# Kernel tuning notes

Measured on AMD Instinct MI355X. Metric: run time of the kernel, lower is better.

Reference implementation:

```python
import jax, jax.numpy as jnp
import numpy as np

D = 256        # d_model
H = 8          # n_heads
L = 4          # n_layers
DFF = 1024     # d_ff = 4*d_model
T = 32768      # total_doms
B = 64         # batch_size (events)
MAX_DOMS = 768 # fixed padded sequence length
NSENS = 5160   # IceCube sensor count


def _layernorm(x, w, b):
    m = x.mean(-1, keepdims=True)
    v = ((x - m) ** 2).mean(-1, keepdims=True)
    return (x - m) * jax.lax.rsqrt(v + 1e-5) * w + b


def _forward(dom_embeddings, geometry, geo_w1, geo_b1, geo_w2, geo_b2,
             qkv_w, qkv_b, out_w, out_b, ln1_w, ln1_b, ln2_w, ln2_b,
             ffn_w1, ffn_b1, ffn_w2, ffn_b2,
             head_w1, head_b1, head_w2, head_b2,
             dom_ids, dom_to_event_idx, batch_size):
    # geometry-aware positional encoding
    geo = geometry[dom_ids] / 500.0                                   # (T,3)
    ge = jax.nn.gelu(geo @ geo_w1.T + geo_b1, approximate=False) @ geo_w2.T + geo_b2
    feat = dom_embeddings + ge                                        # (T,D)

    # pack ragged events -> padded (B, MAX_DOMS, D); dom_to_event_idx is sorted
    total = feat.shape[0]
    counts = jax.ops.segment_sum(jnp.ones((total,), jnp.int32),
                                 dom_to_event_idx, num_segments=batch_size)
    offsets = jnp.cumsum(counts) - counts                              # exclusive prefix
    pos = jnp.arange(total, dtype=jnp.int32) - offsets[dom_to_event_idx]
    x = jnp.zeros((batch_size, MAX_DOMS, D), feat.dtype).at[dom_to_event_idx, pos].set(feat)
    valid = jnp.zeros((batch_size, MAX_DOMS), bool).at[dom_to_event_idx, pos].set(True)
    pad = ~valid                                                       # True for padding

    hd = D // H
    scale = 1.0 / np.sqrt(hd)
    for l in range(L):  # pre-LN transformer encoder (norm_first=True, relu FFN)
        h = _layernorm(x, ln1_w[l], ln1_b[l])
        qkv = h @ qkv_w[l].T + qkv_b[l]                                # (B,S,3D)
        q, k, v = jnp.split(qkv, 3, axis=-1)
        q = q.reshape(batch_size, MAX_DOMS, H, hd)
        k = k.reshape(batch_size, MAX_DOMS, H, hd)
        v = v.reshape(batch_size, MAX_DOMS, H, hd)
        sc = jnp.einsum('bqhd,bkhd->bhqk', q, k) * scale
        sc = jnp.where(pad[:, None, None, :], -1e9, sc)
        a = jax.nn.softmax(sc, axis=-1)
        o = jnp.einsum('bhqk,bkhd->bqhd', a, v).reshape(batch_size, MAX_DOMS, D)
        x = x + o @ out_w[l].T + out_b[l]
        h2 = _layernorm(x, ln2_w[l], ln2_b[l])
        x = x + jax.nn.relu(h2 @ ffn_w1[l].T + ffn_b1[l]) @ ffn_w2[l].T + ffn_b2[l]

    # masked mean pooling
    m = valid[..., None].astype(x.dtype)
    emb = (x * m).sum(axis=1) / jnp.clip(m.sum(axis=1), 1.0)           # (B,D)

    # prediction head + L2 normalization to unit vector
    vec = jax.nn.relu(emb @ head_w1.T + head_b1) @ head_w2.T + head_b2  # (B,3)
    norm = jnp.sqrt(jnp.sum(vec ** 2, axis=1, keepdims=True))
    return vec / (norm + 1e-8)


def setup_inputs() -> dict:
    key = jax.random.key(0)
    ks = jax.random.split(key, 24)
    s = 0.02
    z = jnp.zeros
    inp = {
        'dom_embeddings': jax.random.normal(ks[0], (T, D), jnp.float32),
        'geometry': jax.random.normal(ks[1], (NSENS, 3), jnp.float32) * 300.0,
        'geo_w1': jax.random.normal(ks[2], (D // 2, 3), jnp.float32) * s,
        'geo_b1': z((D // 2,), jnp.float32),
        'geo_w2': jax.random.normal(ks[3], (D, D // 2), jnp.float32) * s,
        'geo_b2': z((D,), jnp.float32),
        'qkv_w': jax.random.normal(ks[4], (L, 3 * D, D), jnp.float32) * s,
        'qkv_b': z((L, 3 * D), jnp.float32),
        'out_w': jax.random.normal(ks[5], (L, D, D), jnp.float32) * s,
        'out_b': z((L, D), jnp.float32),
        'ln1_w': jnp.ones((L, D), jnp.float32), 'ln1_b': z((L, D), jnp.float32),
        'ln2_w': jnp.ones((L, D), jnp.float32), 'ln2_b': z((L, D), jnp.float32),
        'ffn_w1': jax.random.normal(ks[6], (L, DFF, D), jnp.float32) * s,
        'ffn_b1': z((L, DFF), jnp.float32),
        'ffn_w2': jax.random.normal(ks[7], (L, D, DFF), jnp.float32) * s,
        'ffn_b2': z((L, D), jnp.float32),
        'head_w1': jax.random.normal(ks[8], (D, D), jnp.float32) * s,
        'head_b1': z((D,), jnp.float32),
        'head_w2': jax.random.normal(ks[9], (3, D), jnp.float32) * s,
        'head_b2': z((3,), jnp.float32),
        'dom_ids': jax.random.randint(ks[10], (T,), 0, NSENS, jnp.int32),
        'dom_to_event_idx': jnp.sort(jax.random.randint(ks[11], (T,), 0, B, jnp.int32)),
        'batch_size': B,
    }
    return inp


def reference(dom_embeddings, geometry, geo_w1, geo_b1, geo_w2, geo_b2,
              qkv_w, qkv_b, out_w, out_b, ln1_w, ln1_b, ln2_w, ln2_b,
              ffn_w1, ffn_b1, ffn_w2, ffn_b2,
              head_w1, head_b1, head_w2, head_b2,
              dom_ids, dom_to_event_idx, batch_size):
    return _forward(dom_embeddings, geometry, geo_w1, geo_b1, geo_w2, geo_b2,
                    qkv_w, qkv_b, out_w, out_b, ln1_w, ln1_b, ln2_w, ln2_b,
                    ffn_w1, ffn_b1, ffn_w2, ffn_b2,
                    head_w1, head_b1, head_w2, head_b2,
                    dom_ids, dom_to_event_idx, batch_size)
```

## Files before the change

kernel.cpp:

```cpp
#include <hip/hip_runtime.h>
#include <stdint.h>

typedef unsigned short u16;
typedef uint32_t u32;
typedef __bf16 bf16x8 __attribute__((ext_vector_type(8)));
typedef float f32x4 __attribute__((ext_vector_type(4)));

constexpr int T_ = 32768, D_ = 256, H_ = 8, L_ = 4, B_ = 64, NSENS_ = 5160;
constexpr int MGEO_ = 5248;

template <bool Bv> struct bconst { static constexpr bool value = Bv; };

__device__ __forceinline__ u16 f2b(float f) {
  uint32_t u = __builtin_bit_cast(uint32_t, f);
  u += 0x7fffu + ((u >> 16) & 1u);
  return (u16)(u >> 16);
}
__device__ __forceinline__ float fexp2(float x) {
  float r;
  asm("v_exp_f32 %0, %1" : "=v"(r) : "v"(x));
  return r;
}
__device__ __forceinline__ u32 cvtpk(float lo, float hi) {
  u32 r;
  asm("v_cvt_pk_bf16_f32 %0, %1, %2" : "=v"(r) : "v"(lo), "v"(hi));
  return r;
}

__device__ __forceinline__ void gload16(const void* g, void* l) {
  __builtin_amdgcn_global_load_lds(
      (const __attribute__((address_space(1))) void*)g,
      (__attribute__((address_space(3))) void*)l, 16, 0, 0);
}

__global__ void k_offsets(const int* __restrict__ d2e, int* __restrict__ offs) {
  int t = threadIdx.x;
  if (t > B_) return;
  int lo = 0, hi = T_;
  while (lo < hi) { int mid = (lo + hi) >> 1; if (d2e[mid] < t) lo = mid + 1; else hi = mid; }
  offs[t] = lo;
}

__global__ void k_f2b(const float* __restrict__ s, u16* __restrict__ d, int n) {
  int i = blockIdx.x * blockDim.x + threadIdx.x;
  int str = gridDim.x * blockDim.x;
  for (; i < n; i += str) d[i] = f2b(s[i]);
}

__global__ void k_geo1(const float* __restrict__ geom, const float* __restrict__ w1,
                       const float* __restrict__ b1, u16* __restrict__ h1) {
  int i = blockIdx.x * blockDim.x + threadIdx.x;
  if (i >= NSENS_ * 128) return;
  int s = i >> 7, c = i & 127;
  float g0 = geom[s * 3 + 0] * (1.0f / 500.0f);
  float g1 = geom[s * 3 + 1] * (1.0f / 500.0f);
  float g2 = geom[s * 3 + 2] * (1.0f / 500.0f);
  float a = g0 * w1[c * 3 + 0] + g1 * w1[c * 3 + 1] + g2 * w1[c * 3 + 2] + b1[c];
  float g = 0.5f * a * (1.0f + erff(a * 0.70710678118654752f));
  h1[i] = f2b(g);
}

__global__ void k_feat(const float4* __restrict__ de, const float4* __restrict__ ge,
                       const int* __restrict__ dom_ids, float4* __restrict__ x) {
  int i = blockIdx.x * blockDim.x + threadIdx.x;
  if (i >= T_ * 64) return;
  int row = i >> 6, c = i & 63;
  int sid = dom_ids[row];
  float4 a = de[i];
  float4 b = ge[sid * 64 + c];
  float4 o;
  o.x = a.x + b.x; o.y = a.y + b.y; o.z = a.z + b.z; o.w = a.w + b.w;
  x[i] = o;
}

__global__ void k_ln(const float* __restrict__ x, const float* __restrict__ w,
                     const float* __restrict__ b, u16* __restrict__ h) {
  int row = blockIdx.x * 4 + (threadIdx.x >> 6);
  int lane = threadIdx.x & 63;
  const float4 v = *(const float4*)(x + (size_t)row * 256 + lane * 4);
  float s = v.x + v.y + v.z + v.w;
  float q = v.x * v.x + v.y * v.y + v.z * v.z + v.w * v.w;
#pragma unroll
  for (int m = 1; m < 64; m <<= 1) { s += __shfl_xor(s, m); q += __shfl_xor(q, m); }
  float mean = s * (1.0f / 256.0f);
  float var = fmaxf(q * (1.0f / 256.0f) - mean * mean, 0.0f);
  float rs = 1.0f / sqrtf(var + 1e-5f);
  float4 wv = *(const float4*)(w + lane * 4);
  float4 bv = *(const float4*)(b + lane * 4);
  ushort4 o;
  o.x = f2b((v.x - mean) * rs * wv.x + bv.x);
  o.y = f2b((v.y - mean) * rs * wv.y + bv.y);
  o.z = f2b((v.z - mean) * rs * wv.z + bv.z);
  o.w = f2b((v.w - mean) * rs * wv.w + bv.w);
  *(ushort4*)(h + (size_t)row * 256 + lane * 4) = o;
}

template <int EPI>
__global__ __launch_bounds__(256) void k_gemm(const u16* __restrict__ A, const u16* __restrict__ W,
                                              const float* __restrict__ bias, void* __restrict__ out,
                                              int M, int N, int K, int NXB) {
  __shared__ __align__(16) u16 lds[4 * 8192];
  const int nb = gridDim.x;
  const int id = blockIdx.x;
  const int gid = ((nb & 7) == 0) ? ((id & 7) * (nb >> 3) + (id >> 3)) : id;
  const int by = gid / NXB, bx = gid % NXB;
  const int m0 = by * 128, n0 = bx * 128;
  const int tid = threadIdx.x, lane = tid & 63, wv = tid >> 6;
  const int wr = wv >> 1, wc = wv & 1;
  const int l16 = lane & 15, lhi = lane >> 4;
  f32x4 acc[4][4] = {};
  const int NK = K >> 6;

  auto stage = [&](int buf, int kt) {
    char* lbase = (char*)lds + buf * 32768;
#pragma unroll
    for (int c = 0; c < 4; ++c) {
      int pb = c * 4096 + wv * 1024;
      int p = pb + lane * 16;
      int o = p ^ (((p >> 9) & 1) << 5);
      int row = o >> 7, colb = o & 127;
      gload16((const char*)A + ((size_t)(m0 + row) * K) * 2 + kt * 128 + colb, lbase + pb);
      gload16((const char*)W + ((size_t)(n0 + row) * K) * 2 + kt * 128 + colb,
              lbase + 16384 + pb);
    }
  };
  auto compute = [&](int buf) {
    const char* la = (const char*)lds + buf * 32768;
    const char* lb = la + 16384;
#pragma unroll
    for (int ks = 0; ks < 2; ++ks) {
      bf16x8 af[4], bfr[4];
#pragma unroll
      for (int i = 0; i < 4; ++i) {
        int ra = wr * 64 + i * 16 + l16;
        int oa = ra * 128 + ks * 64 + lhi * 16;
        af[i] = *(const bf16x8*)(la + (oa ^ (((oa >> 9) & 1) << 5)));
        int rb = wc * 64 + i * 16 + l16;
        int ob2 = rb * 128 + ks * 64 + lhi * 16;
        bfr[i] = *(const bf16x8*)(lb + (ob2 ^ (((ob2 >> 9) & 1) << 5)));
      }
#pragma unroll
      for (int i = 0; i < 4; ++i)
#pragma unroll
        for (int j = 0; j < 4; ++j)
          acc[i][j] = __builtin_amdgcn_mfma_f32_16x16x32_bf16(af[i], bfr[j], acc[i][j], 0, 0, 0);
    }
  };

  stage(0, 0);
  for (int kt = 0; kt < NK; ++kt) {
    int cur = kt & 1;
    if (kt + 1 < NK) {
      stage(cur ^ 1, kt + 1);
      asm volatile("s_waitcnt vmcnt(8)" ::: "memory");
    } else {
      asm volatile("s_waitcnt vmcnt(0)" ::: "memory");
    }
    __builtin_amdgcn_s_barrier();
    __builtin_amdgcn_sched_barrier(0);
    compute(cur);
    __builtin_amdgcn_sched_barrier(0);
    __builtin_amdgcn_s_barrier();
  }

  float bv[4];
#pragma unroll
  for (int j = 0; j < 4; ++j) bv[j] = bias[n0 + wc * 64 + j * 16 + l16];

  if (EPI <= 1) {
    char* ob_ = (char*)lds;
#pragma unroll
    for (int i = 0; i < 4; ++i)
#pragma unroll
      for (int j = 0; j < 4; ++j)
#pragma unroll
        for (int r = 0; r < 4; ++r) {
          int row = wr * 64 + i * 16 + lhi * 4 + r;
          int col = wc * 64 + j * 16 + l16;
          float v = acc[i][j][r] + bv[j];
          if (EPI == 1) v = fmaxf(v, 0.0f);
          int byte = row * 256 + col * 2;
          *(u16*)(ob_ + (byte ^ ((row & 3) << 5))) = f2b(v);
        }
    __syncthreads();
    int row2 = tid >> 1, half = tid & 1;
    char* dst = (char*)out + ((size_t)(m0 + row2) * N + n0) * 2 + half * 128;
#pragma unroll
    for (int c2 = 0; c2 < 8; ++c2) {
      int byte = row2 * 256 + half * 128 + c2 * 16;
      uint4 t = *(const uint4*)(ob_ + (byte ^ ((row2 & 3) << 5)));
      *(uint4*)(dst + c2 * 16) = t;
    }
  } else {
#pragma unroll
    for (int i = 0; i < 4; ++i)
#pragma unroll
      for (int j = 0; j < 4; ++j)
#pragma unroll
        for (int r = 0; r < 4; ++r) {
          int m = m0 + wr * 64 + i * 16 + lhi * 4 + r;
          int n = n0 + wc * 64 + j * 16 + l16;
          float val = acc[i][j][r] + bv[j];
          if (EPI == 2)
            ((float*)out)[(size_t)m * N + n] += val;
          else
            ((float*)out)[(size_t)m * N + n] = val;
        }
  }
}

__global__ __launch_bounds__(512, 4) void k_attn(const u16* __restrict__ qkv,
                                                 const int* __restrict__ offs,
                                                 u16* __restrict__ ao) {
  const int e = blockIdx.x, qc = blockIdx.y;
  const int off = offs[e], Se = offs[e + 1] - off;
  if (qc * 32 >= Se) return;
  const int tid = threadIdx.x, lane = tid & 63, h = tid >> 6;
  const int l16 = lane & 15, lhi = lane >> 4;

  __shared__ __align__(16) char smem[8 * 5120];
  char* pw = smem + h * 5120;

  bf16x8 qf[2];
#pragma unroll
  for (int qt = 0; qt < 2; ++qt) {
    int qrow = qc * 32 + qt * 16 + l16;
    int g = off + min(qrow, Se - 1);
    qf[qt] = *(const bf16x8*)(qkv + (size_t)g * 768 + h * 32 + lhi * 8);
  }

  f32x4 ob[2][2] = {};
  float m_[2], l_[2];
#pragma unroll
  for (int qt = 0; qt < 2; ++qt) { m_[qt] = -1e30f; l_[qt] = 0.0f; }
  const float SCL2 = 0.25506974760143f;

  auto do_tile = [&](int kb, auto mc) {
    constexpr bool MASK = decltype(mc)::value;
    bf16x8 kf[4];
#pragma unroll
    for (int kt = 0; kt < 4; ++kt) {
      int key = kb + kt * 16 + l16;
      if (MASK) key = min(key, Se - 1);
      kf[kt] = *(const bf16x8*)(qkv + (size_t)(off + key) * 768 + 256 + h * 32 + lhi * 8);
    }
    u16 va0[2][8], va1[2][8];
#pragma unroll
    for (int k2 = 0; k2 < 2; ++k2)
#pragma unroll
      for (int j = 0; j < 8; ++j) {
        int key = kb + k2 * 32 + lhi * 8 + j;
        if (MASK) key = min(key, Se - 1);
        const u16* p = qkv + (size_t)(off + key) * 768 + 512 + h * 32 + l16;
        va0[k2][j] = p[0];
        va1[k2][j] = p[16];
      }
    bf16x8 vf[2][2];
#pragma unroll
    for (int k2 = 0; k2 < 2; ++k2) {
      union { u16 a[8]; bf16x8 v; } u0, u1;
#pragma unroll
      for (int j = 0; j < 8; ++j) { u0.a[j] = va0[k2][j]; u1.a[j] = va1[k2][j]; }
      vf[0][k2] = u0.v;
      vf[1][k2] = u1.v;
    }

#pragma unroll
    for (int qt = 0; qt < 2; ++qt) {
      char* pq = pw + qt * 2304;
      f32x4 sc[4];
      __builtin_amdgcn_s_setprio(1);
#pragma unroll
      for (int kt = 0; kt < 4; ++kt) {
        f32x4 z = {};
        sc[kt] = __builtin_amdgcn_mfma_f32_16x16x32_bf16(kf[kt], qf[qt], z, 0, 0, 0);
      }
      __builtin_amdgcn_s_setprio(0);
      float pv[16], pm = -1e30f;
#pragma unroll
      for (int kt = 0; kt < 4; ++kt)
#pragma unroll
        for (int r = 0; r < 4; ++r) {
          float s = sc[kt][r] * SCL2;
          if (MASK) {
            if (kb + kt * 16 + lhi * 4 + r >= Se) s = -1e30f;
          }
          pv[kt * 4 + r] = s;
          pm = fmaxf(pm, s);
        }
      pm = fmaxf(pm, __shfl_xor(pm, 16));
      pm = fmaxf(pm, __shfl_xor(pm, 32));
      float mn = m_[qt];
      if (!__all(pm <= mn + 11.09f)) {
        mn = fmaxf(mn, pm);
        float csc = fexp2(m_[qt] - mn);
        m_[qt] = mn;
        l_[qt] *= csc;
#pragma unroll
        for (int dt = 0; dt < 2; ++dt)
#pragma unroll
          for (int r = 0; r < 4; ++r) ob[qt][dt][r] *= csc;
      }
      float rs = 0.0f;
#pragma unroll
      for (int i = 0; i < 16; ++i) {
        pv[i] = fexp2(pv[i] - mn);
        rs += pv[i];
      }
      rs += __shfl_xor(rs, 16);
      rs += __shfl_xor(rs, 32);
      l_[qt] += rs;
#pragma unroll
      for (int kt = 0; kt < 4; ++kt)
#pragma unroll
        for (int c = 0; c < 2; ++c)
          *(u32*)(pq + l16 * 144 + (kt * 16 + lhi * 4 + 2 * c) * 2) =
              cvtpk(pv[kt * 4 + 2 * c], pv[kt * 4 + 2 * c + 1]);
      __builtin_amdgcn_s_setprio(1);
#pragma unroll
      for (int k2 = 0; k2 < 2; ++k2) {
        bf16x8 pf = *(const bf16x8*)(pq + l16 * 144 + k2 * 64 + lhi * 16);
#pragma unroll
        for (int dt = 0; dt < 2; ++dt)
          ob[qt][dt] = __builtin_amdgcn_mfma_f32_16x16x32_bf16(vf[dt][k2], pf, ob[qt][dt], 0, 0, 0);
      }
      __builtin_amdgcn_s_setprio(0);
    }
  };

  int kb = 0;
  for (; kb + 64 <= Se; kb += 64) do_tile(kb, bconst<false>{});
  if (kb < Se) do_tile(kb, bconst<true>{});

#pragma unroll
  for (int qt = 0; qt < 2; ++qt) {
    float inv = 1.0f / l_[qt];
#pragma unroll
    for (int dt = 0; dt < 2; ++dt)
#pragma unroll
      for (int c = 0; c < 2; ++c)
        *(u32*)(pw + (qt * 16 + l16) * 80 + (dt * 16 + lhi * 4 + 2 * c) * 2) =
            cvtpk(ob[qt][dt][2 * c] * inv, ob[qt][dt][2 * c + 1] * inv);
  }
  asm volatile("s_waitcnt lgkmcnt(0)" ::: "memory");
  __builtin_amdgcn_sched_barrier(0);
  int qrow = qc * 32 + lane;
  if (lane < 32 && qrow < Se) {
#pragma unroll
    for (int c = 0; c < 4; ++c) {
      uint4 t = *(const uint4*)(pw + lane * 80 + c * 16);
      *(uint4*)((char*)ao + (size_t)(off + qrow) * 512 + h * 64 + c * 16) = t;
    }
  }
}

__global__ void k_pool(const float* __restrict__ x, const int* __restrict__ offs,
                       float* __restrict__ pws) {
  int e = blockIdx.x, s = blockIdx.y, t = threadIdx.x;
  int off = offs[e], cnt = offs[e + 1] - off;
  int r0 = (cnt * s) >> 4, r1 = (cnt * (s + 1)) >> 4;
  float acc = 0.0f;
  for (int r = r0; r < r1; ++r) acc += x[(size_t)(off + r) * 256 + t];
  pws[((e << 4) + s) * 256 + t] = acc;
}

__global__ void k_head(const float* __restrict__ pws, const int* __restrict__ offs,
                       const float* __restrict__ w1, const float* __restrict__ b1,
                       const float* __restrict__ w2, const float* __restrict__ b2,
                       float* __restrict__ out) {
  __shared__ float le[256], hb[256], vec[3];
  int e = blockIdx.x, t = threadIdx.x;
  int cnt = offs[e + 1] - offs[e];
  float acc0 = 0.0f;
#pragma unroll
  for (int s = 0; s < 16; ++s) acc0 += pws[((e << 4) + s) * 256 + t];
  le[t] = acc0 / (float)max(cnt, 1);
  __syncthreads();
  float acc = b1[t];
  const float* wr = w1 + t * 256;
#pragma unroll 8
  for (int k = 0; k < 256; ++k) acc += le[k] * wr[k];
  hb[t] = fmaxf(acc, 0.0f);
  __syncthreads();
  if (t < 3) {
    float a = b2[t];
    const float* w = w2 + t * 256;
    for (int k = 0; k < 256; ++k) a += hb[k] * w[k];
    vec[t] = a;
  }
  __syncthreads();
  if (t < 3) {
    float n = sqrtf(vec[0] * vec[0] + vec[1] * vec[1] + vec[2] * vec[2]);
    out[e * 3 + t] = vec[t] / (n + 1e-8f);
  }
}

extern "C" void kernel_launch(void* const* d_in, const int* in_sizes, int n_in,
                              void* d_out, int out_size, void* d_ws, size_t ws_size,
                              hipStream_t stream) {
  const float* dom_emb = (const float*)d_in[0];
  const float* geometry = (const float*)d_in[1];
  const float* geo_w1 = (const float*)d_in[2];
  const float* geo_b1 = (const float*)d_in[3];
  const float* geo_w2 = (const float*)d_in[4];
  const float* geo_b2 = (const float*)d_in[5];
  const float* qkv_w = (const float*)d_in[6];
  const float* qkv_b = (const float*)d_in[7];
  const float* out_w = (const float*)d_in[8];
  const float* out_b = (const float*)d_in[9];
  const float* ln1_w = (const float*)d_in[10];
  const float* ln1_b = (const float*)d_in[11];
  const float* ln2_w = (const float*)d_in[12];
  const float* ln2_b = (const float*)d_in[13];
  const float* ffn_w1 = (const float*)d_in[14];
  const float* ffn_b1 = (const float*)d_in[15];
  const float* ffn_w2 = (const float*)d_in[16];
  const float* ffn_b2 = (const float*)d_in[17];
  const float* head_w1 = (const float*)d_in[18];
  const float* head_b1 = (const float*)d_in[19];
  const float* head_w2 = (const float*)d_in[20];
  const float* head_b2 = (const float*)d_in[21];
  const int* dom_ids = (const int*)d_in[22];
  const int* d2e = (const int*)d_in[23];

  char* ws = (char*)d_ws;
  constexpr size_t OFF_OFFS = 0;
  constexpr size_t OFF_WBF = 512;
  constexpr size_t OFF_W2B = OFF_WBF + 3145728ull * 2;
  constexpr size_t OFF_H1 = OFF_W2B + 32768ull * 2;
  constexpr size_t OFF_GE = OFF_H1 + (size_t)MGEO_ * 128 * 2;
  constexpr size_t OFF_X = (OFF_GE + (size_t)MGEO_ * 256 * 4 + 255) & ~255ull;
  constexpr size_t OFF_H = OFF_X + (size_t)T_ * 256 * 4;
  constexpr size_t OFF_BIG = OFF_H + (size_t)T_ * 256 * 2;
  constexpr size_t OFF_PWS = OFF_BIG + (size_t)T_ * 1024 * 2;

  int* offs = (int*)(ws + OFF_OFFS);
  u16* wbf = (u16*)(ws + OFF_WBF);
  u16* wbf_qkv = wbf;
  u16* wbf_out = wbf + 786432;
  u16* wbf_f1 = wbf + 1048576;
  u16* wbf_f2 = wbf + 2097152;
  u16* w2b = (u16*)(ws + OFF_W2B);
  u16* h1 = (u16*)(ws + OFF_H1);
  float* ge = (float*)(ws + OFF_GE);
  float* x = (float*)(ws + OFF_X);
  u16* h = (u16*)(ws + OFF_H);
  u16* big = (u16*)(ws + OFF_BIG);
  float* pws = (float*)(ws + OFF_PWS);

  k_offsets<<<1, 128, 0, stream>>>(d2e, offs);
  k_f2b<<<256, 256, 0, stream>>>(qkv_w, wbf_qkv, L_ * 768 * 256);
  k_f2b<<<128, 256, 0, stream>>>(out_w, wbf_out, L_ * 256 * 256);
  k_f2b<<<256, 256, 0, stream>>>(ffn_w1, wbf_f1, L_ * 1024 * 256);
  k_f2b<<<256, 256, 0, stream>>>(ffn_w2, wbf_f2, L_ * 256 * 1024);
  k_f2b<<<32, 256, 0, stream>>>(geo_w2, w2b, 256 * 128);
  k_geo1<<<(NSENS_ * 128 + 255) / 256, 256, 0, stream>>>(geometry, geo_w1, geo_b1, h1);
  k_gemm<3><<<(MGEO_ / 128) * 2, 256, 0, stream>>>(h1, w2b, geo_b2, ge,
                                                   MGEO_, 256, 128, 2);
  k_feat<<<(T_ * 64) / 256, 256, 0, stream>>>((const float4*)dom_emb, (const float4*)ge,
                                              dom_ids, (float4*)x);
  for (int l = 0; l < L_; ++l) {
    k_ln<<<T_ / 4, 256, 0, stream>>>(x, ln1_w + l * 256, ln1_b + l * 256, h);
    k_gemm<0><<<6 * 256, 256, 0, stream>>>(h, wbf_qkv + l * 196608, qkv_b + l * 768,
                                           big, T_, 768, 256, 6);
    k_attn<<<dim3(B_, 24), 512, 0, stream>>>(big, offs, h);
    k_gemm<2><<<2 * 256, 256, 0, stream>>>(h, wbf_out + l * 65536, out_b + l * 256,
                                           x, T_, 256, 256, 2);
    k_ln<<<T_ / 4, 256, 0, stream>>>(x, ln2_w + l * 256, ln2_b + l * 256, h);
    k_gemm<1><<<8 * 256, 256, 0, stream>>>(h, wbf_f1 + l * 262144, ffn_b1 + l * 1024,
                                           big, T_, 1024, 256, 8);
    k_gemm<2><<<2 * 256, 256, 0, stream>>>(big, wbf_f2 + l * 262144, ffn_b2 + l * 256,
                                           x, T_, 256, 1024, 2);
  }
  k_pool<<<dim3(B_, 16), 256, 0, stream>>>(x, offs, pws);
  k_head<<<B_, 256, 0, stream>>>(pws, offs, head_w1, head_b1, head_w2, head_b2, (float*)d_out);
}
```

Measured before the change: 1.019 ms.

## Halve attention query tile to 16 rows and double-buffer K fragment loads

Result: slower. 1.407 ms (+38.0%).

```diff
diff --git a/kernel.cpp b/kernel.cpp
--- a/kernel.cpp
+++ b/kernel.cpp
@@ -214,47 +214,88 @@
                                                  u16* __restrict__ ao) {
   const int e = blockIdx.x, qc = blockIdx.y;
   const int off = offs[e], Se = offs[e + 1] - off;
-  if (qc * 32 >= Se) return;
+  if (qc * 16 >= Se) return;
   const int tid = threadIdx.x, lane = tid & 63, h = tid >> 6;
   const int l16 = lane & 15, lhi = lane >> 4;
 
-  __shared__ __align__(16) char smem[8 * 5120];
-  char* pw = smem + h * 5120;
-
-  bf16x8 qf[2];
-#pragma unroll
-  for (int qt = 0; qt < 2; ++qt) {
-    int qrow = qc * 32 + qt * 16 + l16;
-    int g = off + min(qrow, Se - 1);
-    qf[qt] = *(const bf16x8*)(qkv + (size_t)g * 768 + h * 32 + lhi * 8);
-  }
-
-  f32x4 ob[2][2] = {};
-  float m_[2], l_[2];
-#pragma unroll
-  for (int qt = 0; qt < 2; ++qt) { m_[qt] = -1e30f; l_[qt] = 0.0f; }
+  __shared__ __align__(16) char smem[8 * 4608];
+  char* pw = smem + h * 4608;
+
+  int qrow0 = qc * 16 + l16;
+  int gq = off + min(qrow0, Se - 1);
+  bf16x8 qf = *(const bf16x8*)(qkv + (size_t)gq * 768 + h * 32 + lhi * 8);
+
+  f32x4 ob0 = {}, ob1 = {};
+  float m_ = -1e30f, l_ = 0.0f;
   const float SCL2 = 0.25506974760143f;
 
-  auto do_tile = [&](int kb, auto mc) {
+  auto loadK = [&](int kb, bf16x8 (&kf)[4]) {
+#pragma unroll
+    for (int kt = 0; kt < 4; ++kt) {
+      int key = min(kb + kt * 16 + l16, Se - 1);
+      kf[kt] = *(const bf16x8*)(qkv + (size_t)(off + key) * 768 + 256 + h * 32 + lhi * 8);
+    }
+  };
+
+  auto compute = [&](int kb, int par, bf16x8 (&kf)[4], auto mc) {
     constexpr bool MASK = decltype(mc)::value;
-    bf16x8 kf[4];
-#pragma unroll
-    for (int kt = 0; kt < 4; ++kt) {
-      int key = kb + kt * 16 + l16;
-      if (MASK) key = min(key, Se - 1);
-      kf[kt] = *(const bf16x8*)(qkv + (size_t)(off + key) * 768 + 256 + h * 32 + lhi * 8);
-    }
     u16 va0[2][8], va1[2][8];
 #pragma unroll
     for (int k2 = 0; k2 < 2; ++k2)
 #pragma unroll
       for (int j = 0; j < 8; ++j) {
-        int key = kb + k2 * 32 + lhi * 8 + j;
-        if (MASK) key = min(key, Se - 1);
+        int key = min(kb + k2 * 32 + lhi * 8 + j, Se - 1);
         const u16* p = qkv + (size_t)(off + key) * 768 + 512 + h * 32 + l16;
         va0[k2][j] = p[0];
         va1[k2][j] = p[16];
       }
+    char* pq = pw + par * 2304;
+    f32x4 sc[4];
+    __builtin_amdgcn_s_setprio(1);
+#pragma unroll
+    for (int kt = 0; kt < 4; ++kt) {
+      f32x4 z = {};
+      sc[kt] = __builtin_amdgcn_mfma_f32_16x16x32_bf16(kf[kt], qf, z, 0, 0, 0);
+    }
+    __builtin_amdgcn_s_setprio(0);
+    float pv[16], pm = -1e30f;
+#pragma unroll
+    for (int kt = 0; kt < 4; ++kt)
+#pragma unroll
+      for (int r = 0; r < 4; ++r) {
+        float s = sc[kt][r] * SCL2;
+        if (MASK) {
+          if (kb + kt * 16 + lhi * 4 + r >= Se) s = -1e30f;
+        }
+        pv[kt * 4 + r] = s;
+        pm = fmaxf(pm, s);
+      }
+    pm = fmaxf(pm, __shfl_xor(pm, 16));
+    pm = fmaxf(pm, __shfl_xor(pm, 32));
+    float mn = m_;
+    if (!__all(pm <= mn + 11.09f)) {
+      mn = fmaxf(mn, pm);
+      float csc = fexp2(m_ - mn);
+      m_ = mn;
+      l_ *= csc;
+#pragma unroll
+      for (int r = 0; r < 4; ++r) { ob0[r] *= csc; ob1[r] *= csc; }
+    }
+    float rs = 0.0f;
+#pragma unroll
+    for (int i = 0; i < 16; ++i) {
+      pv[i] = fexp2(pv[i] - mn);
+      rs += pv[i];
+    }
+    rs += __shfl_xor(rs, 16);
+    rs += __shfl_xor(rs, 32);
+    l_ += rs;
+#pragma unroll
+    for (int kt = 0; kt < 4; ++kt)
+#pragma unroll
+      for (int c = 0; c < 2; ++c)
+        *(u32*)(pq + l16 * 144 + (kt * 16 + lhi * 4 + 2 * c) * 2) =
+            cvtpk(pv[kt * 4 + 2 * c], pv[kt * 4 + 2 * c + 1]);
     bf16x8 vf[2][2];
 #pragma unroll
     for (int k2 = 0; k2 < 2; ++k2) {
@@ -264,92 +305,58 @@
       vf[0][k2] = u0.v;
       vf[1][k2] = u1.v;
     }
-
-#pragma unroll
-    for (int qt = 0; qt < 2; ++qt) {
-      char* pq = pw + qt * 2304;
-      f32x4 sc[4];
-      __builtin_amdgcn_s_setprio(1);
-#pragma unroll
-      for (int kt = 0; kt < 4; ++kt) {
-        f32x4 z = {};
-        sc[kt] = __builtin_amdgcn_mfma_f32_16x16x32_bf16(kf[kt], qf[qt], z, 0, 0, 0);
-      }
-      __builtin_amdgcn_s_setprio(0);
-      float pv[16], pm = -1e30f;
-#pragma unroll
-      for (int kt = 0; kt < 4; ++kt)
-#pragma unroll
-        for (int r = 0; r < 4; ++r) {
-          float s = sc[kt][r] * SCL2;
-          if (MASK) {
-            if (kb + kt * 16 + lhi * 4 + r >= Se) s = -1e30f;
-          }
-          pv[kt * 4 + r] = s;
-          pm = fmaxf(pm, s);
-        }
-      pm = fmaxf(pm, __shfl_xor(pm, 16));
-      pm = fmaxf(pm, __shfl_xor(pm, 32));
-      float mn = m_[qt];
-      if (!__all(pm <= mn + 11.09f)) {
-        mn = fmaxf(mn, pm);
-        float csc = fexp2(m_[qt] - mn);
-        m_[qt] = mn;
-        l_[qt] *= csc;
-#pragma unroll
-        for (int dt = 0; dt < 2; ++dt)
-#pragma unroll
-          for (int r = 0; r < 4; ++r) ob[qt][dt][r] *= csc;
-      }
-      float rs = 0.0f;
-#pragma unroll
-      for (int i = 0; i < 16; ++i) {
-        pv[i] = fexp2(pv[i] - mn);
-        rs += pv[i];
-      }
-      rs += __shfl_xor(rs, 16);
-      rs += __shfl_xor(rs, 32);
-      l_[qt] += rs;
-#pragma unroll
-      for (int kt = 0; kt < 4; ++kt)
-#pragma unroll
-        for (int c = 0; c < 2; ++c)
-          *(u32*)(pq + l16 * 144 + (kt * 16 + lhi * 4 + 2 * c) * 2) =
-              cvtpk(pv[kt * 4 + 2 * c], pv[kt * 4 + 2 * c + 1]);
-      __builtin_amdgcn_s_setprio(1);
-#pragma unroll
-      for (int k2 = 0; k2 < 2; ++k2) {
-        bf16x8 pf = *(const bf16x8*)(pq + l16 * 144 + k2 * 64 + lhi * 16);
-#pragma unroll
-        for (int dt = 0; dt < 2; ++dt)
-          ob[qt][dt] = __builtin_amdgcn_mfma_f32_16x16x32_bf16(vf[dt][k2], pf, ob[qt][dt], 0, 0, 0);
-      }
-      __builtin_amdgcn_s_setprio(0);
-    }
+    __builtin_amdgcn_s_setprio(1);
+#pragma unroll
+    for (int k2 = 0; k2 < 2; ++k2) {
+      bf16x8 pf = *(const bf16x8*)(pq + l16 * 144 + k2 * 64 + lhi * 16);
+      ob0 = __builtin_amdgcn_mfma_f32_16x16x32_bf16(vf[0][k2], pf, ob0, 0, 0, 0);
+      ob1 = __builtin_amdgcn_mfma_f32_16x16x32_bf16(vf[1][k2], pf, ob1, 0, 0, 0);
+    }
+    __builtin_amdgcn_s_setprio(0);
   };
 
-  int kb = 0;
-  for (; kb + 64 <= Se; kb += 64) do_tile(kb, bconst<false>{});
-  if (kb < Se) do_tile(kb, bconst<true>{});
-
-#pragma unroll
-  for (int qt = 0; qt < 2; ++qt) {
-    float inv = 1.0f / l_[qt];
-#pragma unroll
-    for (int dt = 0; dt < 2; ++dt)
-#pragma unroll
-      for (int c = 0; c < 2; ++c)
-        *(u32*)(pw + (qt * 16 + l16) * 80 + (dt * 16 + lhi * 4 + 2 * c) * 2) =
-            cvtpk(ob[qt][dt][2 * c] * inv, ob[qt][dt][2 * c + 1] * inv);
+  const int nt = (Se + 63) >> 6;
+  const bool tail = (Se & 63) != 0;
+  bf16x8 kfA[4], kfB[4];
+  loadK(0, kfA);
+  int t = 0;
+  for (;;) {
+    if (t + 1 < nt) loadK((t + 1) << 6, kfB);
+    if (t == nt - 1) {
+      if (tail) compute(t << 6, t & 1, kfA, bconst<true>{});
+      else      compute(t << 6, t & 1, kfA, bconst<false>{});
+      break;
+    }
+    compute(t << 6, t & 1, kfA, bconst<false>{});
+    ++t;
+    if (t + 1 < nt) loadK((t + 1) << 6, kfA);
+    if (t == nt - 1) {
+      if (tail) compute(t << 6, t & 1, kfB, bconst<true>{});
+      else      compute(t << 6, t & 1, kfB, bconst<false>{});
+      break;
+    }
+    compute(t << 6, t & 1, kfB, bconst<false>{});
+    ++t;
+  }
+
+  {
+    float inv = 1.0f / l_;
+#pragma unroll
+    for (int c = 0; c < 2; ++c) {
+      *(u32*)(pw + l16 * 80 + (lhi * 4 + 2 * c) * 2) =
+          cvtpk(ob0[2 * c] * inv, ob0[2 * c + 1] * inv);
+      *(u32*)(pw + l16 * 80 + (16 + lhi * 4 + 2 * c) * 2) =
+          cvtpk(ob1[2 * c] * inv, ob1[2 * c + 1] * inv);
+    }
   }
   asm volatile("s_waitcnt lgkmcnt(0)" ::: "memory");
   __builtin_amdgcn_sched_barrier(0);
-  int qrow = qc * 32 + lane;
-  if (lane < 32 && qrow < Se) {
+  int qrow = qc * 16 + lane;
+  if (lane < 16 && qrow < Se) {
 #pragma unroll
     for (int c = 0; c < 4; ++c) {
-      uint4 t = *(const uint4*)(pw + lane * 80 + c * 16);
-      *(uint4*)((char*)ao + (size_t)(off + qrow) * 512 + h * 64 + c * 16) = t;
+      uint4 t4 = *(const uint4*)(pw + lane * 80 + c * 16);
+      *(uint4*)((char*)ao + (size_t)(off + qrow) * 512 + h * 64 + c * 16) = t4;
     }
   }
 }
@@ -463,7 +470,7 @@
     k_ln<<<T_ / 4, 256, 0, stream>>>(x, ln1_w + l * 256, ln1_b + l * 256, h);
     k_gemm<0><<<6 * 256, 256, 0, stream>>>(h, wbf_qkv + l * 196608, qkv_b + l * 768,
                                            big, T_, 768, 256, 6);
-    k_attn<<<dim3(B_, 24), 512, 0, stream>>>(big, offs, h);
+    k_attn<<<dim3(B_, 48), 512, 0, stream>>>(big, offs, h);
     k_gemm<2><<<2 * 256, 256, 0, stream>>>(h, wbf_out + l * 65536, out_b + l * 256,
                                            x, T_, 256, 256, 2);
     k_ln<<<T_ / 4, 256, 0, stream>>>(x, ln2_w + l * 256, ln2_b + l * 256, h);
```

## Fuse LayerNorm into residual GEMM epilogues and feature-add kernel

Applied to the files above, without the earlier changes.

Result: faster. 906.1 us (-11.1%).

```diff
diff --git a/kernel.cpp b/kernel.cpp
--- a/kernel.cpp
+++ b/kernel.cpp
@@ -60,24 +60,18 @@
   h1[i] = f2b(g);
 }
 
-__global__ void k_feat(const float4* __restrict__ de, const float4* __restrict__ ge,
-                       const int* __restrict__ dom_ids, float4* __restrict__ x) {
-  int i = blockIdx.x * blockDim.x + threadIdx.x;
-  if (i >= T_ * 64) return;
-  int row = i >> 6, c = i & 63;
-  int sid = dom_ids[row];
-  float4 a = de[i];
-  float4 b = ge[sid * 64 + c];
-  float4 o;
-  o.x = a.x + b.x; o.y = a.y + b.y; o.z = a.z + b.z; o.w = a.w + b.w;
-  x[i] = o;
-}
-
-__global__ void k_ln(const float* __restrict__ x, const float* __restrict__ w,
-                     const float* __restrict__ b, u16* __restrict__ h) {
+__global__ void k_featln(const float4* __restrict__ de, const float4* __restrict__ ge,
+                         const int* __restrict__ dom_ids, const float* __restrict__ w,
+                         const float* __restrict__ b, float4* __restrict__ x,
+                         u16* __restrict__ h) {
   int row = blockIdx.x * 4 + (threadIdx.x >> 6);
   int lane = threadIdx.x & 63;
-  const float4 v = *(const float4*)(x + (size_t)row * 256 + lane * 4);
+  int sid = dom_ids[row];
+  float4 a = de[row * 64 + lane];
+  float4 g = ge[sid * 64 + lane];
+  float4 v;
+  v.x = a.x + g.x; v.y = a.y + g.y; v.z = a.z + g.z; v.w = a.w + g.w;
+  x[row * 64 + lane] = v;
   float s = v.x + v.y + v.z + v.w;
   float q = v.x * v.x + v.y * v.y + v.z * v.z + v.w * v.w;
 #pragma unroll
@@ -207,6 +201,139 @@
             ((float*)out)[(size_t)m * N + n] = val;
         }
   }
+}
+
+__global__ __launch_bounds__(256) void k_gemm_ln(const u16* __restrict__ A,
+                                                 const u16* __restrict__ W,
+                                                 const float* __restrict__ bias,
+                                                 const float* __restrict__ lnw,
+                                                 const float* __restrict__ lnb,
+                                                 float* __restrict__ x,
+                                                 u16* __restrict__ hout, int K) {
+  __shared__ __align__(16) u16 lds[2 * 20480];
+  const int nb = gridDim.x;
+  const int id = blockIdx.x;
+  const int gid = (id & 7) * (nb >> 3) + (id >> 3);
+  const int m0 = gid * 64;
+  const int tid = threadIdx.x, lane = tid & 63, wv = tid >> 6;
+  const int l16 = lane & 15, lhi = lane >> 4;
+  f32x4 acc[4][4] = {};
+  const int NK = K >> 6;
+
+  auto stage = [&](int buf, int kt) {
+    char* lbase = (char*)lds + buf * 40960;
+#pragma unroll
+    for (int c = 0; c < 10; ++c) {
+      int pb = c * 4096 + wv * 1024;
+      int p, reg;
+      if (pb < 8192) { p = pb; reg = 0; } else { p = pb - 8192; reg = 1; }
+      int pl = p + lane * 16;
+      int o = pl ^ (((pl >> 9) & 1) << 5);
+      int row = o >> 7, colb = o & 127;
+      const char* src = reg == 0
+          ? (const char*)A + ((size_t)(m0 + row) * K) * 2 + kt * 128 + colb
+          : (const char*)W + ((size_t)row * K) * 2 + kt * 128 + colb;
+      gload16(src, lbase + (reg ? 8192 : 0) + p);
+    }
+  };
+  auto compute = [&](int buf) {
+    const char* la = (const char*)lds + buf * 40960;
+    const char* lb = la + 8192;
+#pragma unroll
+    for (int ks = 0; ks < 2; ++ks) {
+      bf16x8 af[4], bfr[4];
+#pragma unroll
+      for (int i = 0; i < 4; ++i) {
+        int oa = (i * 16 + l16) * 128 + ks * 64 + lhi * 16;
+        af[i] = *(const bf16x8*)(la + (oa ^ (((oa >> 9) & 1) << 5)));
+        int ob2 = (wv * 64 + i * 16 + l16) * 128 + ks * 64 + lhi * 16;
+        bfr[i] = *(const bf16x8*)(lb + (ob2 ^ (((ob2 >> 9) & 1) << 5)));
+      }
+#pragma unroll
+      for (int i = 0; i < 4; ++i)
+#pragma unroll
+        for (int j = 0; j < 4; ++j)
+          acc[i][j] = __builtin_amdgcn_mfma_f32_16x16x32_bf16(af[i], bfr[j], acc[i][j], 0, 0, 0);
+    }
+  };
+
+  stage(0, 0);
+  for (int kt = 0; kt < NK; ++kt) {
+    int cur = kt & 1;
+    if (kt + 1 < NK) {
+      stage(cur ^ 1, kt + 1);
+      asm volatile("s_waitcnt vmcnt(10)" ::: "memory");
+    } else {
+      asm volatile("s_waitcnt vmcnt(0)" ::: "memory");
+    }
+    __builtin_amdgcn_s_barrier();
+    __builtin_amdgcn_sched_barrier(0);
+    compute(cur);
+    __builtin_amdgcn_sched_barrier(0);
+    __builtin_amdgcn_s_barrier();
+  }
+
+  float bv[4], wl[4], bl[4];
+#pragma unroll
+  for (int j = 0; j < 4; ++j) {
+    int col = wv * 64 + j * 16 + l16;
+    bv[j] = bias[col];
+    wl[j] = lnw[col];
+    bl[j] = lnb[col];
+  }
+#pragma unroll
+  for (int i = 0; i < 4; ++i)
+#pragma unroll
+    for (int r = 0; r < 4; ++r) {
+      int row = i * 16 + lhi * 4 + r;
+#pragma unroll
+      for (int j = 0; j < 4; ++j) {
+        int col = wv * 64 + j * 16 + l16;
+        acc[i][j][r] += bv[j] + x[(size_t)(m0 + row) * 256 + col];
+      }
+    }
+  float* lr = (float*)lds;
+  __syncthreads();
+#pragma unroll
+  for (int i = 0; i < 4; ++i)
+#pragma unroll
+    for (int r = 0; r < 4; ++r) {
+      float s = 0.0f, q = 0.0f;
+#pragma unroll
+      for (int j = 0; j < 4; ++j) { float v = acc[i][j][r]; s += v; q += v * v; }
+#pragma unroll
+      for (int m = 1; m < 16; m <<= 1) { s += __shfl_xor(s, m); q += __shfl_xor(q, m); }
+      if (l16 == 0) {
+        int row = i * 16 + lhi * 4 + r;
+        lr[wv * 64 + row] = s;
+        lr[256 + wv * 64 + row] = q;
+      }
+    }
+  __syncthreads();
+  if (tid < 64) {
+    float s = lr[tid] + lr[64 + tid] + lr[128 + tid] + lr[192 + tid];
+    float q = lr[256 + tid] + lr[320 + tid] + lr[384 + tid] + lr[448 + tid];
+    float mean = s * (1.0f / 256.0f);
+    float var = fmaxf(q * (1.0f / 256.0f) - mean * mean, 0.0f);
+    lr[512 + tid * 2] = mean;
+    lr[512 + tid * 2 + 1] = 1.0f / sqrtf(var + 1e-5f);
+  }
+  __syncthreads();
+#pragma unroll
+  for (int i = 0; i < 4; ++i)
+#pragma unroll
+    for (int r = 0; r < 4; ++r) {
+      int row = i * 16 + lhi * 4 + r;
+      float mean = lr[512 + row * 2];
+      float rstd = lr[512 + row * 2 + 1];
+#pragma unroll
+      for (int j = 0; j < 4; ++j) {
+        int col = wv * 64 + j * 16 + l16;
+        float v = acc[i][j][r];
+        x[(size_t)(m0 + row) * 256 + col] = v;
+        hout[(size_t)(m0 + row) * 256 + col] = f2b((v - mean) * rstd * wl[j] + bl[j]);
+      }
+    }
 }
 
 __global__ __launch_bounds__(512, 4) void k_attn(const u16* __restrict__ qkv,
@@ -457,20 +584,24 @@
   k_geo1<<<(NSENS_ * 128 + 255) / 256, 256, 0, stream>>>(geometry, geo_w1, geo_b1, h1);
   k_gemm<3><<<(MGEO_ / 128) * 2, 256, 0, stream>>>(h1, w2b, geo_b2, ge,
                                                    MGEO_, 256, 128, 2);
-  k_feat<<<(T_ * 64) / 256, 256, 0, stream>>>((const float4*)dom_emb, (const float4*)ge,
-                                              dom_ids, (float4*)x);
+  k_featln<<<T_ / 4, 256, 0, stream>>>((const float4*)dom_emb, (const float4*)ge,
+                                       dom_ids, ln1_w, ln1_b, (float4*)x, h);
   for (int l = 0; l < L_; ++l) {
-    k_ln<<<T_ / 4, 256, 0, stream>>>(x, ln1_w + l * 256, ln1_b + l * 256, h);
     k_gemm<0><<<6 * 256, 256, 0, stream>>>(h, wbf_qkv + l * 196608, qkv_b + l * 768,
                                            big, T_, 768, 256, 6);
     k_attn<<<dim3(B_, 24), 512, 0, stream>>>(big, offs, h);
-    k_gemm<2><<<2 * 256, 256, 0, stream>>>(h, wbf_out + l * 65536, out_b + l * 256,
-                                           x, T_, 256, 256, 2);
-    k_ln<<<T_ / 4, 256, 0, stream>>>(x, ln2_w + l * 256, ln2_b + l * 256, h);
+    k_gemm_ln<<<T_ / 64, 256, 0, stream>>>(h, wbf_out + l * 65536, out_b + l * 256,
+                                           ln2_w + l * 256, ln2_b + l * 256, x, h, 256);
     k_gemm<1><<<8 * 256, 256, 0, stream>>>(h, wbf_f1 + l * 262144, ffn_b1 + l * 1024,
                                            big, T_, 1024, 256, 8);
-    k_gemm<2><<<2 * 256, 256, 0, stream>>>(big, wbf_f2 + l * 262144, ffn_b2 + l * 256,
-                                           x, T_, 256, 1024, 2);
+    if (l < L_ - 1) {
+      k_gemm_ln<<<T_ / 64, 256, 0, stream>>>(big, wbf_f2 + l * 262144, ffn_b2 + l * 256,
+                                             ln1_w + (l + 1) * 256, ln1_b + (l + 1) * 256,
+                                             x, h, 1024);
+    } else {
+      k_gemm<2><<<2 * 256, 256, 0, stream>>>(big, wbf_f2 + l * 262144, ffn_b2 + l * 256,
+                                             x, T_, 256, 1024, 2);
+    }
   }
   k_pool<<<dim3(B_, 16), 256, 0, stream>>>(x, offs, pws);
   k_head<<<B_, 256, 0, stream>>>(pws, offs, head_w1, head_b1, head_w2, head_b2, (float*)d_out);
```
